# Performance work log

Measured on AMD Instinct MI355X. Metric: run time of the kernel, lower is better.

Reference implementation:

```python
import jax, jax.numpy as jnp
import numpy as np

D = 256
H = 8
HD = D // H  # 32
EPS = 1e-5


def _ln(x, g, b):
    m = jnp.mean(x, axis=-1, keepdims=True)
    v = jnp.var(x, axis=-1, keepdims=True)
    return (x - m) * jax.lax.rsqrt(v + EPS) * g + b


def setup_inputs() -> dict:
    key = jax.random.key(0)
    ks = jax.random.split(key, 30)
    B = 131072
    s = 0.05

    def w(k, shape, scale=s):
        return jax.random.normal(k, shape, dtype=jnp.float32) * scale

    inp = {
        'f24': w(ks[0], (B, D), 1.0),
        'f77': w(ks[1], (B, D), 1.0),
        'fx': w(ks[2], (B, D), 1.0),
        'norm_g': jnp.ones((D,), jnp.float32),
        'norm_b': jnp.zeros((D,), jnp.float32),
        'Wq24': w(ks[3], (D, D)), 'bq24': w(ks[4], (D,)),
        'Wk24': w(ks[5], (D, D)), 'bk24': w(ks[6], (D,)),
        'Wv24': w(ks[7], (D, D)), 'bv24': w(ks[8], (D,)),
        'Wq77': w(ks[9], (D, D)), 'bq77': w(ks[10], (D,)),
        'Wk77': w(ks[11], (D, D)), 'bk77': w(ks[12], (D,)),
        'Wv77': w(ks[13], (D, D)), 'bv77': w(ks[14], (D,)),
        'Wqx': w(ks[15], (D, D)), 'bqx': w(ks[16], (D,)),
        'Wkx': w(ks[17], (D, D)), 'bkx': w(ks[18], (D,)),
        'Wvx': w(ks[19], (D, D)), 'bvx': w(ks[20], (D,)),
        'Wout': w(ks[21], (D, D)), 'bout': w(ks[22], (D,)),
        'radar_w': jnp.ones((3,), jnp.float32),
        'W1': w(ks[23], (D, 4 * D)), 'b1': w(ks[24], (4 * D,)),
        'W2': w(ks[25], (4 * D, D)), 'b2': w(ks[26], (D,)),
        'fnorm_g': jnp.ones((D,), jnp.float32),
        'fnorm_b': jnp.zeros((D,), jnp.float32),
    }
    return inp


def reference(f24, f77, fx, norm_g, norm_b,
              Wq24, bq24, Wk24, bk24, Wv24, bv24,
              Wq77, bq77, Wk77, bk77, Wv77, bv77,
              Wqx, bqx, Wkx, bkx, Wvx, bvx,
              Wout, bout, radar_w, W1, b1, W2, b2,
              fnorm_g, fnorm_b):
    B = f24.shape[0]
    residual = (f24 + f77 + fx) / 3.0
    n24 = _ln(f24, norm_g, norm_b)
    n77 = _ln(f77, norm_g, norm_b)
    nx = _ln(fx, norm_g, norm_b)

    def proj(x, W, b):
        return (x @ W + b).reshape(B, H, HD)

    q24 = proj(n24, Wq24, bq24); k24 = proj(n24, Wk24, bk24); v24 = proj(n24, Wv24, bv24)
    q77 = proj(n77, Wq77, bq77); k77 = proj(n77, Wk77, bk77); v77 = proj(n77, Wv77, bv77)
    qx = proj(nx, Wqx, bqx); kx = proj(nx, Wkx, bkx); vx = proj(nx, Wvx, bvx)

    scale = HD ** (-0.5)

    def att(q, ka, kb):  # [B,H,H] each
        a = jnp.einsum('bhd,bgd->bhg', q, ka) * scale
        b_ = jnp.einsum('bhd,bgd->bhg', q, kb) * scale
        # softmax across the two radar sources (stacked dim), NOT over keys
        return jax.nn.softmax(jnp.stack([a, b_], axis=1), axis=1)

    attn_24 = att(q24, k77, kx)
    attn_77 = att(q77, k24, kx)
    attn_x = att(qx, k24, k77)

    def mix(p, va, vb):  # [B,2,H,H] x [B,H,HD] -> [B, D]
        o = jnp.einsum('bhg,bgd->bhd', p[:, 0], va) + jnp.einsum('bhg,bgd->bhd', p[:, 1], vb)
        return o.reshape(B, D)

    out_24 = mix(attn_24, v77, vx)
    out_77 = mix(attn_77, v24, vx)
    out_x = mix(attn_x, v24, v77)

    rw = jax.nn.softmax(radar_w, axis=0)
    fused = rw[0] * out_24 + rw[1] * out_77 + rw[2] * out_x
    fused = fused @ Wout + bout
    fused = fused + residual
    ff = jax.nn.gelu(fused @ W1 + b1, approximate=False) @ W2 + b2  # dropout = eval identity
    output = _ln(fused + ff, fnorm_g, fnorm_b)
    return output, rw
```

## Files before the change

### kernel.cpp

```cpp
#include <hip/hip_runtime.h>

#define DEV __device__ __forceinline__

typedef float f4_t __attribute__((ext_vector_type(4)));
typedef short v8s  __attribute__((ext_vector_type(8)));

DEV float lo16(unsigned int w){ return __uint_as_float(w << 16); }
DEV float hi16(unsigned int w){ return __uint_as_float(w & 0xffff0000u); }
DEV float b2f(unsigned short u){ return __uint_as_float((unsigned)u << 16); }
DEV unsigned short f2b(float f){
  unsigned int x = __float_as_uint(f);
  x += 0x7fffu + ((x >> 16) & 1u);
  return (unsigned short)(x >> 16);
}
DEV float geluf(float v){ return 0.5f * v * (1.0f + erff(v * 0.7071067811865475f)); }

DEV void gload_lds16(const unsigned short* g, unsigned short* l){
  __builtin_amdgcn_global_load_lds(
      (const __attribute__((address_space(1))) void*)g,
      (__attribute__((address_space(3))) void*)l, 16, 0, 0);
}

#define WAITV(n) asm volatile("s_waitcnt vmcnt(" #n ")" ::: "memory")
#define SBAR()  do{ __builtin_amdgcn_sched_barrier(0); \
                    asm volatile("s_barrier" ::: "memory"); \
                    __builtin_amdgcn_sched_barrier(0); }while(0)

__global__ void k_prep(
    const float* Wq24, const float* Wk24, const float* Wv24,
    const float* Wq77, const float* Wk77, const float* Wv77,
    const float* Wqx,  const float* Wkx,  const float* Wvx,
    const float* bq24, const float* bk24, const float* bv24,
    const float* bq77, const float* bk77, const float* bv77,
    const float* bqx,  const float* bkx,  const float* bvx,
    const float* Wout, const float* W1,   const float* W2,
    const float* radar_w,
    unsigned short* wt_cat, unsigned short* wout_t,
    unsigned short* w1_t, unsigned short* w2_t,
    float* bias_cat, float* rwbuf, float* out_tail)
{
  long idx = (long)blockIdx.x * blockDim.x + threadIdx.x;
  if (idx < 589824){
    int s = (int)(idx / 196608);
    int r = (int)(idx % 196608);
    int ng = r >> 8, k = r & 255;
    int which = ng >> 8, n = ng & 255;
    const float* src;
    switch (s*3 + which){
      case 0: src = Wq24; break;  case 1: src = Wk24; break;  case 2: src = Wv24; break;
      case 3: src = Wq77; break;  case 4: src = Wk77; break;  case 5: src = Wv77; break;
      case 6: src = Wqx;  break;  case 7: src = Wkx;  break;  default: src = Wvx; break;
    }
    wt_cat[idx] = f2b(src[k*256 + n]);
    return;
  }
  idx -= 589824;
  if (idx < 65536){ int n = (int)(idx >> 8), k = (int)(idx & 255);
    wout_t[idx] = f2b(Wout[k*256 + n]); return; }
  idx -= 65536;
  if (idx < 262144){ int n = (int)(idx >> 8), k = (int)(idx & 255);
    w1_t[idx] = f2b(W1[k*1024 + n]); return; }
  idx -= 262144;
  if (idx < 262144){ int n = (int)(idx >> 10), k = (int)(idx & 1023);
    w2_t[idx] = f2b(W2[k*256 + n]); return; }
  idx -= 262144;
  if (idx < 2304){
    int s = (int)(idx / 768), j = (int)(idx % 768);
    int which = j >> 8, jj = j & 255;
    const float* src;
    switch (s*3 + which){
      case 0: src = bq24; break;  case 1: src = bk24; break;  case 2: src = bv24; break;
      case 3: src = bq77; break;  case 4: src = bk77; break;  case 5: src = bv77; break;
      case 6: src = bqx;  break;  case 7: src = bkx;  break;  default: src = bvx; break;
    }
    bias_cat[idx] = src[jj]; return;
  }
  idx -= 2304;
  if (idx < 3){
    float w0 = radar_w[0], w1v = radar_w[1], w2v = radar_w[2];
    float m = fmaxf(w0, fmaxf(w1v, w2v));
    float e0 = __expf(w0-m), e1 = __expf(w1v-m), e2 = __expf(w2v-m);
    float inv = 1.0f/(e0+e1+e2);
    float rw = (idx==0 ? e0 : (idx==1 ? e1 : e2)) * inv;
    rwbuf[idx] = rw; out_tail[idx] = rw;
  }
}

__global__ __launch_bounds__(256) void k_ln3(
    const float* __restrict__ f24, const float* __restrict__ f77, const float* __restrict__ fx,
    const float* __restrict__ gg, const float* __restrict__ bb,
    unsigned short* __restrict__ nbuf, float* __restrict__ resid, int rows)
{
  int wid = threadIdx.x >> 6, lane = threadIdx.x & 63;
  long row = (long)blockIdx.x*4 + wid;
  long base = row*256 + lane*4;
  f4_t x0 = *(const f4_t*)(f24 + base);
  f4_t x1 = *(const f4_t*)(f77 + base);
  f4_t x2 = *(const f4_t*)(fx  + base);
  float s[3], q[3];
  s[0]=x0.x+x0.y+x0.z+x0.w;
  s[1]=x1.x+x1.y+x1.z+x1.w;
  s[2]=x2.x+x2.y+x2.z+x2.w;
  q[0]=fmaf(x0.x,x0.x,fmaf(x0.y,x0.y,fmaf(x0.z,x0.z,x0.w*x0.w)));
  q[1]=fmaf(x1.x,x1.x,fmaf(x1.y,x1.y,fmaf(x1.z,x1.z,x1.w*x1.w)));
  q[2]=fmaf(x2.x,x2.x,fmaf(x2.y,x2.y,fmaf(x2.z,x2.z,x2.w*x2.w)));
  #pragma unroll
  for (int m=1;m<64;m<<=1){
    #pragma unroll
    for (int j=0;j<3;j++){ s[j]+=__shfl_xor(s[j],m); q[j]+=__shfl_xor(q[j],m); }
  }
  f4_t G  = *(const f4_t*)(gg + lane*4);
  f4_t Bv = *(const f4_t*)(bb + lane*4);
  long strm = (long)rows*256;
  {
    float mean = s[0]*(1.0f/256.0f);
    float rstd = rsqrtf(q[0]*(1.0f/256.0f) - mean*mean + 1e-5f);
    ushort4 o;
    o.x=f2b((x0.x-mean)*rstd*G.x+Bv.x); o.y=f2b((x0.y-mean)*rstd*G.y+Bv.y);
    o.z=f2b((x0.z-mean)*rstd*G.z+Bv.z); o.w=f2b((x0.w-mean)*rstd*G.w+Bv.w);
    *(ushort4*)(nbuf + base) = o;
  }
  {
    float mean = s[1]*(1.0f/256.0f);
    float rstd = rsqrtf(q[1]*(1.0f/256.0f) - mean*mean + 1e-5f);
    ushort4 o;
    o.x=f2b((x1.x-mean)*rstd*G.x+Bv.x); o.y=f2b((x1.y-mean)*rstd*G.y+Bv.y);
    o.z=f2b((x1.z-mean)*rstd*G.z+Bv.z); o.w=f2b((x1.w-mean)*rstd*G.w+Bv.w);
    *(ushort4*)(nbuf + strm + base) = o;
  }
  {
    float mean = s[2]*(1.0f/256.0f);
    float rstd = rsqrtf(q[2]*(1.0f/256.0f) - mean*mean + 1e-5f);
    ushort4 o;
    o.x=f2b((x2.x-mean)*rstd*G.x+Bv.x); o.y=f2b((x2.y-mean)*rstd*G.y+Bv.y);
    o.z=f2b((x2.z-mean)*rstd*G.z+Bv.z); o.w=f2b((x2.w-mean)*rstd*G.w+Bv.w);
    *(ushort4*)(nbuf + 2*strm + base) = o;
  }
  f4_t rs;
  rs.x=(x0.x+x1.x+x2.x)*(1.0f/3.0f);
  rs.y=(x0.y+x1.y+x2.y)*(1.0f/3.0f);
  rs.z=(x0.z+x1.z+x2.z)*(1.0f/3.0f);
  rs.w=(x0.w+x1.w+x2.w)*(1.0f/3.0f);
  *(f4_t*)(resid + base) = rs;
}

template<int EPI>
__global__ __launch_bounds__(256,2) void k_gemm256(
    const unsigned short* __restrict__ A, const unsigned short* __restrict__ Bt,
    const float* __restrict__ bias,
    unsigned short* __restrict__ outH,
    long aBatch, long bBatch, long biasBatch, long oBatch, int ldOut,
    int tM, int tN, int tZ)
{
  __shared__ __align__(16) unsigned short As[2][128][64];
  __shared__ __align__(16) unsigned short Bs[2][128][64];
  int tid = threadIdx.x, wid = tid >> 6, lane = tid & 63;
  int wm = (wid >> 1)*64, wn = (wid & 1)*64;
  int lr = lane & 15, lk = lane >> 4;

  int total = tM*tN*tZ;
  int nT = (total - (int)blockIdx.x + (int)gridDim.x - 1) / (int)gridDim.x;
  if (nT <= 0) return;
  int G = nT*4;

  auto tileOf = [&](int j, long& m0, int& n0, int& z){
    int T = (int)blockIdx.x + j*(int)gridDim.x;
    int mt = T % tM; int rest = T / tM;
    int nt = rest % tN; z = rest / tN;
    m0 = (long)mt*128; n0 = nt*128;
  };

  auto stage = [&](int g){
    long m0; int n0, z;
    tileOf(g >> 2, m0, n0, z);
    int k0 = (g & 3)*64, bi = g & 1;
    const unsigned short* Ab = A  + (long)z*aBatch + m0*256;
    const unsigned short* Bb = Bt + (long)z*bBatch + (long)n0*256;
    #pragma unroll
    for (int i=0;i<4;i++){
      int c = (wid*4+i)*64 + lane;
      int r = c >> 3, sl = (c & 7) ^ (r & 7);
      gload_lds16(Ab + (long)r*256 + k0 + sl*8, &As[bi][0][0] + (long)(wid*4+i)*512);
      gload_lds16(Bb + (long)r*256 + k0 + sl*8, &Bs[bi][0][0] + (long)(wid*4+i)*512);
    }
  };

  const f4_t fz = {0.f,0.f,0.f,0.f};
  f4_t acc[4][4] = {};

  stage(0);
  for (int g=0; g<G; ++g){
    if (g+1 < G){ stage(g+1); WAITV(8); }
    else        { WAITV(0); }
    SBAR();
    int cur = g & 1;
    #pragma unroll
    for (int ks=0; ks<2; ++ks){
      v8s af[4], bfv[4];
      #pragma unroll
      for (int f=0; f<4; f++){
        int prA = wm + f*16 + lr;
        int prB = wn + f*16 + lr;
        int js  = ks*4 + lk;
        af[f]  = *(const v8s*)&As[cur][prA][(js ^ (prA & 7))*8];
        bfv[f] = *(const v8s*)&Bs[cur][prB][(js ^ (prB & 7))*8];
      }
      #pragma unroll
      for (int fm=0; fm<4; fm++)
        #pragma unroll
        for (int fn=0; fn<4; fn++)
          acc[fm][fn] = __builtin_amdgcn_mfma_f32_16x16x32_bf16(bfv[fn], af[fm], acc[fm][fn], 0,0,0);
    }
    if ((g & 3) == 3){
      long m0; int n0, z;
      tileOf(g >> 2, m0, n0, z);
      long zo = (long)z*oBatch;
      const float* bp = bias + (long)z*biasBatch;
      #pragma unroll
      for (int fm=0; fm<4; fm++){
        long gm = m0 + wm + fm*16 + lr;
        long rowo = zo + gm*(long)ldOut;
        #pragma unroll
        for (int fn=0; fn<4; fn++){
          int gn = n0 + wn + fn*16 + lk*4;
          f4_t bv = *(const f4_t*)(bp + gn);
          f4_t v = acc[fm][fn];
          v.x += bv.x; v.y += bv.y; v.z += bv.z; v.w += bv.w;
          ushort4 o; o.x=f2b(v.x); o.y=f2b(v.y); o.z=f2b(v.z); o.w=f2b(v.w);
          *(ushort4*)(outH + rowo + gn) = o;
          acc[fm][fn] = fz;
        }
      }
    }
    SBAR();
  }
}

__global__ __launch_bounds__(512,4) void k_attn(
    const unsigned short* __restrict__ qkv, const float* __restrict__ rwb,
    unsigned short* __restrict__ outA, int rows)
{
  __shared__ __align__(16) unsigned short L[8][72][40];
  int tid = threadIdx.x, wid = tid >> 6, lane = tid & 63;
  long brow0 = (long)blockIdx.x * 8;
  for (int c = tid; c < 2304; c += 512){
    int row = c / 288, rem = c % 288;
    int s = rem / 96, cc = rem % 96;
    int vi = cc >> 2, ch = cc & 3;
    const uint4* src = (const uint4*)(qkv + ((long)s*rows + brow0 + row)*768 + cc*8);
    *(uint4*)&L[row][s*24 + vi][ch*8] = *src;
  }
  __syncthreads();

  int h = lane >> 3, g = lane & 7;
  const unsigned short* R = &L[wid][0][0];
  float comb[32];
  #pragma unroll
  for (int i=0;i<32;i++) comb[i] = 0.0f;
  float rw0 = rwb[0], rw1 = rwb[1], rw2 = rwb[2];

  #pragma unroll
  for (int att=0; att<3; ++att){
    int qs  = att;
    int as_ = (att==0) ? 1 : 0;
    int bs_ = (att==2) ? 1 : 2;
    float rwv = (att==0) ? rw0 : ((att==1) ? rw1 : rw2);
    const unsigned short* qp  = R + (qs *24      + h)*40;
    const unsigned short* kap = R + (as_*24 + 8  + g)*40;
    const unsigned short* kbp = R + (bs_*24 + 8  + g)*40;
    float a = 0.0f, b = 0.0f;
    #pragma unroll
    for (int j=0;j<4;j++){
      uint4 qc  = *(const uint4*)(qp  + j*8);
      uint4 kac = *(const uint4*)(kap + j*8);
      uint4 kbc = *(const uint4*)(kbp + j*8);
      #define DOT2(QW,KA,KB) { float q0=lo16(QW), q1=hi16(QW); \
        a=fmaf(q0,lo16(KA),a); a=fmaf(q1,hi16(KA),a); \
        b=fmaf(q0,lo16(KB),b); b=fmaf(q1,hi16(KB),b); }
      DOT2(qc.x, kac.x, kbc.x) DOT2(qc.y, kac.y, kbc.y)
      DOT2(qc.z, kac.z, kbc.z) DOT2(qc.w, kac.w, kbc.w)
      #undef DOT2
    }
    float d  = (b - a) * 0.17677669529663689f;
    float p0 = 1.0f / (1.0f + __expf(d));
    float p1 = 1.0f - p0;
    float w0 = rwv * p0, w1 = rwv * p1;
    const unsigned short* vap = R + (as_*24 + 16 + g)*40;
    const unsigned short* vbp = R + (bs_*24 + 16 + g)*40;
    #pragma unroll
    for (int j=0;j<4;j++){
      uint4 va = *(const uint4*)(vap + j*8);
      uint4 vb = *(const uint4*)(vbp + j*8);
      #define MIX2(VA,VB,C0,C1) { \
        C0 = fmaf(w0, lo16(VA), fmaf(w1, lo16(VB), C0)); \
        C1 = fmaf(w0, hi16(VA), fmaf(w1, hi16(VB), C1)); }
      MIX2(va.x, vb.x, comb[j*8+0], comb[j*8+1])
      MIX2(va.y, vb.y, comb[j*8+2], comb[j*8+3])
      MIX2(va.z, vb.z, comb[j*8+4], comb[j*8+5])
      MIX2(va.w, vb.w, comb[j*8+6], comb[j*8+7])
      #undef MIX2
    }
  }

  float t16[16];
  { bool up = (lane & 4) != 0;
    #pragma unroll
    for (int i=0;i<16;i++){
      float send = up ? comb[i] : comb[16+i];
      float keep = up ? comb[16+i] : comb[i];
      t16[i] = keep + __shfl_xor(send, 4);
    } }
  float t8[8];
  { bool up = (lane & 2) != 0;
    #pragma unroll
    for (int i=0;i<8;i++){
      float send = up ? t16[i] : t16[8+i];
      float keep = up ? t16[8+i] : t16[i];
      t8[i] = keep + __shfl_xor(send, 2);
    } }
  float t4[4];
  { bool up = (lane & 1) != 0;
    #pragma unroll
    for (int i=0;i<4;i++){
      float send = up ? t8[i] : t8[4+i];
      float keep = up ? t8[4+i] : t8[i];
      t4[i] = keep + __shfl_xor(send, 1);
    } }

  long orow = brow0 + wid;
  ushort4 o4;
  o4.x = f2b(t4[0]); o4.y = f2b(t4[1]); o4.z = f2b(t4[2]); o4.w = f2b(t4[3]);
  *(ushort4*)(outA + orow*256 + lane*4) = o4;
}

__global__ __launch_bounds__(256,2) void k_back(
    const unsigned short* __restrict__ attn,
    const float* __restrict__ resid,
    const unsigned short* __restrict__ woutT,
    const unsigned short* __restrict__ w1T,
    const unsigned short* __restrict__ w2T,
    const float* __restrict__ bout, const float* __restrict__ b1,
    const float* __restrict__ b2,
    const float* __restrict__ fg, const float* __restrict__ fb,
    float* __restrict__ dout)
{
  __shared__ __align__(16) unsigned short FL[8192];
  __shared__ __align__(16) unsigned short STG[16384];
  __shared__ __align__(16) unsigned short R2[4096];
  int tid = threadIdx.x, wid = tid >> 6, lane = tid & 63;
  int lr = lane & 15, lk = lane >> 4;
  int wn = wid*64, wnB = wid*32;
  long m0 = (long)blockIdx.x * 32;

  f4_t accA[2][4] = {};
  for (int t=0; t<4; ++t){
    { int c = tid; int r = c>>3, sl = (c&7)^(r&7);
      gload_lds16(attn + (m0+r)*256 + t*64 + sl*8, R2 + c*8); }
    #pragma unroll
    for (int i=0;i<8;i++){ int c = i*256+tid; int r = c>>3, sl = (c&7)^(r&7);
      gload_lds16(woutT + (long)r*256 + t*64 + sl*8, STG + c*8); }
    __syncthreads();
    #pragma unroll
    for (int ks=0; ks<2; ++ks){
      v8s af[2], bf[4];
      #pragma unroll
      for (int f=0; f<2; f++){ int pr = f*16+lr;
        af[f] = *(const v8s*)(R2 + pr*64 + (((ks*4+lk) ^ (pr&7))*8)); }
      #pragma unroll
      for (int f=0; f<4; f++){ int pr = wn + f*16 + lr;
        bf[f] = *(const v8s*)(STG + pr*64 + (((ks*4+lk) ^ (pr&7))*8)); }
      #pragma unroll
      for (int fm=0; fm<2; fm++)
        #pragma unroll
        for (int fn=0; fn<4; fn++)
          accA[fm][fn] = __builtin_amdgcn_mfma_f32_16x16x32_bf16(bf[fn], af[fm], accA[fm][fn], 0,0,0);
    }
    __syncthreads();
  }
  #pragma unroll
  for (int fm=0; fm<2; fm++){
    int row = fm*16 + lr;
    #pragma unroll
    for (int fn=0; fn<4; fn++){
      int col = wn + fn*16 + lk*4;
      f4_t bv = *(const f4_t*)(bout + col);
      f4_t rv = *(const f4_t*)(resid + (m0+row)*256 + col);
      f4_t v = accA[fm][fn];
      v.x += bv.x + rv.x; v.y += bv.y + rv.y; v.z += bv.z + rv.z; v.w += bv.w + rv.w;
      ushort4 hh; hh.x=f2b(v.x); hh.y=f2b(v.y); hh.z=f2b(v.z); hh.w=f2b(v.w);
      int us = row*256 + (((col>>3) ^ (row&7))*8) + (col&7);
      *(ushort4*)(FL + us) = hh;
    }
  }
  __syncthreads();

  f4_t acc2[2][4] = {};
  for (int s=0; s<8; ++s){
    f4_t accH[2][2] = {};
    for (int t=0; t<4; ++t){
      #pragma unroll
      for (int i=0;i<4;i++){ int c = i*256+tid; int r = c>>3, sl = (c&7)^(r&7);
        gload_lds16(w1T + (long)(s*128+r)*256 + t*64 + sl*8, STG + c*8); }
      __syncthreads();
      #pragma unroll
      for (int ks=0; ks<2; ++ks){
        v8s af[2], bf[2];
        #pragma unroll
        for (int f=0; f<2; f++){ int pr = f*16+lr; int ku = t*8 + ks*4 + lk;
          af[f] = *(const v8s*)(FL + pr*256 + ((ku ^ (pr&7))*8)); }
        #pragma unroll
        for (int f=0; f<2; f++){ int pr = wnB + f*16 + lr;
          bf[f] = *(const v8s*)(STG + pr*64 + (((ks*4+lk) ^ (pr&7))*8)); }
        #pragma unroll
        for (int fm=0; fm<2; fm++)
          #pragma unroll
          for (int fn=0; fn<2; fn++)
            accH[fm][fn] = __builtin_amdgcn_mfma_f32_16x16x32_bf16(bf[fn], af[fm], accH[fm][fn], 0,0,0);
      }
      __syncthreads();
    }
    #pragma unroll
    for (int fm=0; fm<2; fm++){
      int row = fm*16 + lr;
      #pragma unroll
      for (int fn=0; fn<2; fn++){
        int col = wnB + fn*16 + lk*4;
        f4_t bv = *(const f4_t*)(b1 + s*128 + col);
        f4_t v = accH[fm][fn];
        v.x = geluf(v.x+bv.x); v.y = geluf(v.y+bv.y);
        v.z = geluf(v.z+bv.z); v.w = geluf(v.w+bv.w);
        ushort4 hh; hh.x=f2b(v.x); hh.y=f2b(v.y); hh.z=f2b(v.z); hh.w=f2b(v.w);
        int us = row*128 + (((col>>3) ^ (row&7))*8) + (col&7);
        *(ushort4*)(R2 + us) = hh;
      }
    }
    __syncthreads();
    for (int t=0; t<2; ++t){
      #pragma unroll
      for (int i=0;i<8;i++){ int c = i*256+tid; int r = c>>3, sl = (c&7)^(r&7);
        gload_lds16(w2T + (long)r*1024 + s*128 + t*64 + sl*8, STG + c*8); }
      __syncthreads();
      #pragma unroll
      for (int ks=0; ks<2; ++ks){
        v8s af[2], bf[4];
        #pragma unroll
        for (int f=0; f<2; f++){ int pr = f*16+lr; int ku = t*8 + ks*4 + lk;
          af[f] = *(const v8s*)(R2 + pr*128 + ((ku ^ (pr&7))*8)); }
        #pragma unroll
        for (int f=0; f<4; f++){ int pr = wn + f*16 + lr;
          bf[f] = *(const v8s*)(STG + pr*64 + (((ks*4+lk) ^ (pr&7))*8)); }
        #pragma unroll
        for (int fm=0; fm<2; fm++)
          #pragma unroll
          for (int fn=0; fn<4; fn++)
            acc2[fm][fn] = __builtin_amdgcn_mfma_f32_16x16x32_bf16(bf[fn], af[fm], acc2[fm][fn], 0,0,0);
      }
      __syncthreads();
    }
  }

  f4_t vv[2][4];
  float ps[2], pq[2];
  #pragma unroll
  for (int fm=0; fm<2; fm++){
    int row = fm*16 + lr;
    ps[fm] = 0.0f; pq[fm] = 0.0f;
    #pragma unroll
    for (int fn=0; fn<4; fn++){
      int col = wn + fn*16 + lk*4;
      f4_t bv = *(const f4_t*)(b2 + col);
      int us = row*256 + (((col>>3) ^ (row&7))*8) + (col&7);
      ushort4 fh = *(const ushort4*)(FL + us);
      f4_t v = acc2[fm][fn];
      v.x += bv.x + b2f(fh.x); v.y += bv.y + b2f(fh.y);
      v.z += bv.z + b2f(fh.z); v.w += bv.w + b2f(fh.w);
      vv[fm][fn] = v;
      ps[fm] += v.x+v.y+v.z+v.w;
      pq[fm] += v.x*v.x + v.y*v.y + v.z*v.z + v.w*v.w;
    }
    ps[fm] += __shfl_xor(ps[fm], 16); ps[fm] += __shfl_xor(ps[fm], 32);
    pq[fm] += __shfl_xor(pq[fm], 16); pq[fm] += __shfl_xor(pq[fm], 32);
  }
  float* PS = (float*)R2;
  float* PQ = (float*)R2 + 128;
  if (lk == 0){
    #pragma unroll
    for (int fm=0; fm<2; fm++){ int row = fm*16+lr;
      PS[row*4 + wid] = ps[fm]; PQ[row*4 + wid] = pq[fm]; }
  }
  __syncthreads();
  #pragma unroll
  for (int fm=0; fm<2; fm++){
    int row = fm*16 + lr;
    f4_t sv = *(const f4_t*)(PS + row*4);
    f4_t qv = *(const f4_t*)(PQ + row*4);
    float S = sv.x+sv.y+sv.z+sv.w, Q = qv.x+qv.y+qv.z+qv.w;
    float mean = S*(1.0f/256.0f);
    float rstd = rsqrtf(Q*(1.0f/256.0f) - mean*mean + 1e-5f);
    #pragma unroll
    for (int fn=0; fn<4; fn++){
      int col = wn + fn*16 + lk*4;
      f4_t G = *(const f4_t*)(fg + col);
      f4_t Bb = *(const f4_t*)(fb + col);
      f4_t v = vv[fm][fn], o;
      o.x = (v.x-mean)*rstd*G.x + Bb.x;
      o.y = (v.y-mean)*rstd*G.y + Bb.y;
      o.z = (v.z-mean)*rstd*G.z + Bb.z;
      o.w = (v.w-mean)*rstd*G.w + Bb.w;
      *(f4_t*)(dout + (m0+row)*256 + col) = o;
    }
  }
}

extern "C" void kernel_launch(void* const* d_in, const int* in_sizes, int n_in,
                              void* d_out, int out_size, void* d_ws, size_t ws_size,
                              hipStream_t stream)
{
  const float* f24    = (const float*)d_in[0];
  const float* f77    = (const float*)d_in[1];
  const float* fx     = (const float*)d_in[2];
  const float* norm_g = (const float*)d_in[3];
  const float* norm_b = (const float*)d_in[4];
  const float* Wq24 = (const float*)d_in[5];  const float* bq24 = (const float*)d_in[6];
  const float* Wk24 = (const float*)d_in[7];  const float* bk24 = (const float*)d_in[8];
  const float* Wv24 = (const float*)d_in[9];  const float* bv24 = (const float*)d_in[10];
  const float* Wq77 = (const float*)d_in[11]; const float* bq77 = (const float*)d_in[12];
  const float* Wk77 = (const float*)d_in[13]; const float* bk77 = (const float*)d_in[14];
  const float* Wv77 = (const float*)d_in[15]; const float* bv77 = (const float*)d_in[16];
  const float* Wqx  = (const float*)d_in[17]; const float* bqx  = (const float*)d_in[18];
  const float* Wkx  = (const float*)d_in[19]; const float* bkx  = (const float*)d_in[20];
  const float* Wvx  = (const float*)d_in[21]; const float* bvx  = (const float*)d_in[22];
  const float* Wout = (const float*)d_in[23]; const float* bout = (const float*)d_in[24];
  const float* radar_w = (const float*)d_in[25];
  const float* W1 = (const float*)d_in[26];   const float* b1 = (const float*)d_in[27];
  const float* W2 = (const float*)d_in[28];   const float* b2 = (const float*)d_in[29];
  const float* fnorm_g = (const float*)d_in[30];
  const float* fnorm_b = (const float*)d_in[31];

  const long Brows = (long)in_sizes[0] / 256;
  float* dout = (float*)d_out;
  char* ws = (char*)d_ws;

  size_t off = 0;
  auto A_ = [&](size_t b){ size_t o = off; off = (off + b + 255) & ~(size_t)255; return o; };
  size_t oWT = A_((size_t)3*768*256*2);
  size_t oWO = A_((size_t)65536*2);
  size_t oW1 = A_((size_t)262144*2);
  size_t oW2 = A_((size_t)262144*2);
  size_t oBC = A_((size_t)2304*4);
  size_t oRW = A_(256);
  size_t fixedEnd = off;

  unsigned short* WT_CAT = (unsigned short*)(ws + oWT);
  unsigned short* WOUT_T = (unsigned short*)(ws + oWO);
  unsigned short* W1_T   = (unsigned short*)(ws + oW1);
  unsigned short* W2_T   = (unsigned short*)(ws + oW2);
  float*          BIASC  = (float*)(ws + oBC);
  float*          RW     = (float*)(ws + oRW);

  const size_t PER_ROW = 7168;
  if (ws_size <= fixedEnd + 512) return;
  long maxR = (long)((ws_size - fixedEnd - 256) / PER_ROW);
  maxR &= ~127L;
  if (maxR < 128) return;
  long Rc = maxR < 65536 ? maxR : 65536;
  if (Rc > Brows) Rc = Brows;
  long nch = (Brows + Rc - 1) / Rc;
  Rc = ((Brows + nch - 1) / nch + 127) & ~127L;

  size_t chunkBase = (fixedEnd + 255) & ~(size_t)255;
  char* NB_B = ws + chunkBase;
  char* RS_B = NB_B + (size_t)1536*Rc;
  char* QK_B = RS_B + (size_t)1024*Rc;

  {
    long total = 589824 + 65536 + 262144 + 262144 + 2304 + 3;
    int blocks = (int)((total + 255) / 256);
    k_prep<<<blocks, 256, 0, stream>>>(
        Wq24, Wk24, Wv24, Wq77, Wk77, Wv77, Wqx, Wkx, Wvx,
        bq24, bk24, bv24, bq77, bk77, bv77, bqx, bkx, bvx,
        Wout, W1, W2, radar_w,
        WT_CAT, WOUT_T, W1_T, W2_T, BIASC, RW, dout + (size_t)Brows*256);
  }

  for (long row0 = 0; row0 < Brows; row0 += Rc){
    long rows = Brows - row0 < Rc ? Brows - row0 : Rc;
    unsigned short* NBUF   = (unsigned short*)NB_B;
    float*          RESID  = (float*)RS_B;
    unsigned short* QKV    = (unsigned short*)QK_B;
    unsigned short* ATTN   = (unsigned short*)NB_B;

    int tM = (int)(rows/128);

    k_ln3<<<(int)(rows/4), 256, 0, stream>>>(
        f24 + row0*256, f77 + row0*256, fx + row0*256,
        norm_g, norm_b, NBUF, RESID, (int)rows);

    { int tiles = tM*6*3; int grid = tiles < 512 ? tiles : 512;
      k_gemm256<0><<<grid, 256, 0, stream>>>(
          NBUF, WT_CAT, BIASC, QKV,
          rows*256L, 768L*256, 768L, rows*768L, 768, tM, 6, 3); }

    k_attn<<<(int)(rows/8), 512, 0, stream>>>(QKV, RW, ATTN, (int)rows);

    k_back<<<(int)(rows/32), 256, 0, stream>>>(
        ATTN, RESID, WOUT_T, W1_T, W2_T,
        bout, b1, b2, fnorm_g, fnorm_b, dout + row0*256);
  }
}
```

Measured before the change: 1.613 ms.

## Make attention kernel persistent with double-buffered async LDS staging, shrink chunk size

The attention kernel becomes a persistent grid-stride loop over 8-row tiles, capped at 512 blocks. It double-buffers tiles in LDS using async global_load_lds so the next tile loads while the current one is computed. The LDS row padding is removed to fit two buffers, and the dot products now use split accumulators. The host row chunk shrinks from 65536 to 16384 rows, which may improve L2 residency of intermediates but adds more launches, and the unpadded layout may cause LDS bank conflicts.

Result: faster. 1.405 ms (-12.9%).

```diff
diff --git a/kernel.cpp b/kernel.cpp
--- a/kernel.cpp
+++ b/kernel.cpp
@@ -240,97 +240,121 @@
     const unsigned short* __restrict__ qkv, const float* __restrict__ rwb,
     unsigned short* __restrict__ outA, int rows)
 {
-  __shared__ __align__(16) unsigned short L[8][72][40];
+  __shared__ __align__(16) unsigned short L[2][8][72][32];
   int tid = threadIdx.x, wid = tid >> 6, lane = tid & 63;
-  long brow0 = (long)blockIdx.x * 8;
-  for (int c = tid; c < 2304; c += 512){
-    int row = c / 288, rem = c % 288;
-    int s = rem / 96, cc = rem % 96;
-    int vi = cc >> 2, ch = cc & 3;
-    const uint4* src = (const uint4*)(qkv + ((long)s*rows + brow0 + row)*768 + cc*8);
-    *(uint4*)&L[row][s*24 + vi][ch*8] = *src;
-  }
-  __syncthreads();
-
+  int nT = rows >> 3;
+  int t0 = blockIdx.x;
+  if (t0 >= nT) return;
+
+  auto stage = [&](int b, int tile){
+    long brow0 = (long)tile*8;
+    unsigned short* Lb = &L[b][0][0][0];
+    #pragma unroll
+    for (int it=0; it<5; ++it){
+      int cw = it*512 + wid*64;
+      if (cw < 2304){
+        int c = cw + lane;
+        int row = c/288, rem = c - row*288;
+        int s = rem/96,  cc  = rem - s*96;
+        gload_lds16(qkv + ((long)s*rows + brow0 + row)*768 + cc*8,
+                    Lb + (long)cw*8);
+      }
+    }
+  };
+
+  float rw0 = rwb[0], rw1 = rwb[1], rw2 = rwb[2];
   int h = lane >> 3, g = lane & 7;
-  const unsigned short* R = &L[wid][0][0];
-  float comb[32];
-  #pragma unroll
-  for (int i=0;i<32;i++) comb[i] = 0.0f;
-  float rw0 = rwb[0], rw1 = rwb[1], rw2 = rwb[2];
-
-  #pragma unroll
-  for (int att=0; att<3; ++att){
-    int qs  = att;
-    int as_ = (att==0) ? 1 : 0;
-    int bs_ = (att==2) ? 1 : 2;
-    float rwv = (att==0) ? rw0 : ((att==1) ? rw1 : rw2);
-    const unsigned short* qp  = R + (qs *24      + h)*40;
-    const unsigned short* kap = R + (as_*24 + 8  + g)*40;
-    const unsigned short* kbp = R + (bs_*24 + 8  + g)*40;
-    float a = 0.0f, b = 0.0f;
-    #pragma unroll
-    for (int j=0;j<4;j++){
-      uint4 qc  = *(const uint4*)(qp  + j*8);
-      uint4 kac = *(const uint4*)(kap + j*8);
-      uint4 kbc = *(const uint4*)(kbp + j*8);
-      #define DOT2(QW,KA,KB) { float q0=lo16(QW), q1=hi16(QW); \
-        a=fmaf(q0,lo16(KA),a); a=fmaf(q1,hi16(KA),a); \
-        b=fmaf(q0,lo16(KB),b); b=fmaf(q1,hi16(KB),b); }
-      DOT2(qc.x, kac.x, kbc.x) DOT2(qc.y, kac.y, kbc.y)
-      DOT2(qc.z, kac.z, kbc.z) DOT2(qc.w, kac.w, kbc.w)
-      #undef DOT2
-    }
-    float d  = (b - a) * 0.17677669529663689f;
-    float p0 = 1.0f / (1.0f + __expf(d));
-    float p1 = 1.0f - p0;
-    float w0 = rwv * p0, w1 = rwv * p1;
-    const unsigned short* vap = R + (as_*24 + 16 + g)*40;
-    const unsigned short* vbp = R + (bs_*24 + 16 + g)*40;
-    #pragma unroll
-    for (int j=0;j<4;j++){
-      uint4 va = *(const uint4*)(vap + j*8);
-      uint4 vb = *(const uint4*)(vbp + j*8);
-      #define MIX2(VA,VB,C0,C1) { \
-        C0 = fmaf(w0, lo16(VA), fmaf(w1, lo16(VB), C0)); \
-        C1 = fmaf(w0, hi16(VA), fmaf(w1, hi16(VB), C1)); }
-      MIX2(va.x, vb.x, comb[j*8+0], comb[j*8+1])
-      MIX2(va.y, vb.y, comb[j*8+2], comb[j*8+3])
-      MIX2(va.z, vb.z, comb[j*8+4], comb[j*8+5])
-      MIX2(va.w, vb.w, comb[j*8+6], comb[j*8+7])
-      #undef MIX2
-    }
-  }
-
-  float t16[16];
-  { bool up = (lane & 4) != 0;
-    #pragma unroll
-    for (int i=0;i<16;i++){
-      float send = up ? comb[i] : comb[16+i];
-      float keep = up ? comb[16+i] : comb[i];
-      t16[i] = keep + __shfl_xor(send, 4);
-    } }
-  float t8[8];
-  { bool up = (lane & 2) != 0;
-    #pragma unroll
-    for (int i=0;i<8;i++){
-      float send = up ? t16[i] : t16[8+i];
-      float keep = up ? t16[8+i] : t16[i];
-      t8[i] = keep + __shfl_xor(send, 2);
-    } }
-  float t4[4];
-  { bool up = (lane & 1) != 0;
-    #pragma unroll
-    for (int i=0;i<4;i++){
-      float send = up ? t8[i] : t8[4+i];
-      float keep = up ? t8[4+i] : t8[i];
-      t4[i] = keep + __shfl_xor(send, 1);
-    } }
-
-  long orow = brow0 + wid;
-  ushort4 o4;
-  o4.x = f2b(t4[0]); o4.y = f2b(t4[1]); o4.z = f2b(t4[2]); o4.w = f2b(t4[3]);
-  *(ushort4*)(outA + orow*256 + lane*4) = o4;
+
+  stage(0, t0);
+  int pb = 0;
+  for (int t = t0; t < nT; t += (int)gridDim.x){
+    SBAR();
+    int tn = t + (int)gridDim.x;
+    if (tn < nT){ stage(pb^1, tn); WAITV(5); }
+    else        { WAITV(0); }
+    SBAR();
+
+    const unsigned short* R = &L[pb][wid][0][0];
+    float comb[32];
+    #pragma unroll
+    for (int i=0;i<32;i++) comb[i] = 0.0f;
+
+    #pragma unroll
+    for (int att=0; att<3; ++att){
+      int qs  = att;
+      int as_ = (att==0) ? 1 : 0;
+      int bs_ = (att==2) ? 1 : 2;
+      float rwv = (att==0) ? rw0 : ((att==1) ? rw1 : rw2);
+      const unsigned short* qp  = R + (qs *24      + h)*32;
+      const unsigned short* kap = R + (as_*24 + 8  + g)*32;
+      const unsigned short* kbp = R + (bs_*24 + 8  + g)*32;
+      float a0=0.f, a1=0.f, b0=0.f, b1=0.f;
+      #pragma unroll
+      for (int j=0;j<4;j++){
+        uint4 qc  = *(const uint4*)(qp  + j*8);
+        uint4 kac = *(const uint4*)(kap + j*8);
+        uint4 kbc = *(const uint4*)(kbp + j*8);
+        float* ap = (j&1) ? &a1 : &a0;
+        float* bp = (j&1) ? &b1 : &b0;
+        #define DOT2(QW,KA,KB) { float q0=lo16(QW), q1=hi16(QW); \
+          *ap=fmaf(q0,lo16(KA),*ap); *ap=fmaf(q1,hi16(KA),*ap); \
+          *bp=fmaf(q0,lo16(KB),*bp); *bp=fmaf(q1,hi16(KB),*bp); }
+        DOT2(qc.x, kac.x, kbc.x) DOT2(qc.y, kac.y, kbc.y)
+        DOT2(qc.z, kac.z, kbc.z) DOT2(qc.w, kac.w, kbc.w)
+        #undef DOT2
+      }
+      float d  = ((b0+b1) - (a0+a1)) * 0.17677669529663689f;
+      float p0 = 1.0f / (1.0f + __expf(d));
+      float p1 = 1.0f - p0;
+      float w0 = rwv * p0, w1 = rwv * p1;
+      const unsigned short* vap = R + (as_*24 + 16 + g)*32;
+      const unsigned short* vbp = R + (bs_*24 + 16 + g)*32;
+      #pragma unroll
+      for (int j=0;j<4;j++){
+        uint4 va = *(const uint4*)(vap + j*8);
+        uint4 vb = *(const uint4*)(vbp + j*8);
+        #define MIX2(VA,VB,C0,C1) { \
+          C0 = fmaf(w0, lo16(VA), fmaf(w1, lo16(VB), C0)); \
+          C1 = fmaf(w0, hi16(VA), fmaf(w1, hi16(VB), C1)); }
+        MIX2(va.x, vb.x, comb[j*8+0], comb[j*8+1])
+        MIX2(va.y, vb.y, comb[j*8+2], comb[j*8+3])
+        MIX2(va.z, vb.z, comb[j*8+4], comb[j*8+5])
+        MIX2(va.w, vb.w, comb[j*8+6], comb[j*8+7])
+        #undef MIX2
+      }
+    }
+
+    float t16[16];
+    { bool up = (lane & 4) != 0;
+      #pragma unroll
+      for (int i=0;i<16;i++){
+        float send = up ? comb[i] : comb[16+i];
+        float keep = up ? comb[16+i] : comb[i];
+        t16[i] = keep + __shfl_xor(send, 4);
+      } }
+    float t8[8];
+    { bool up = (lane & 2) != 0;
+      #pragma unroll
+      for (int i=0;i<8;i++){
+        float send = up ? t16[i] : t16[8+i];
+        float keep = up ? t16[8+i] : t16[i];
+        t8[i] = keep + __shfl_xor(send, 2);
+      } }
+    float t4[4];
+    { bool up = (lane & 1) != 0;
+      #pragma unroll
+      for (int i=0;i<4;i++){
+        float send = up ? t8[i] : t8[4+i];
+        float keep = up ? t8[4+i] : t8[i];
+        t4[i] = keep + __shfl_xor(send, 1);
+      } }
+
+    long orow = (long)t*8 + wid;
+    ushort4 o4;
+    o4.x = f2b(t4[0]); o4.y = f2b(t4[1]); o4.z = f2b(t4[2]); o4.w = f2b(t4[3]);
+    *(ushort4*)(outA + orow*256 + lane*4) = o4;
+    pb ^= 1;
+  }
 }
 
 __global__ __launch_bounds__(256,2) void k_back(
@@ -563,7 +587,7 @@
   long maxR = (long)((ws_size - fixedEnd - 256) / PER_ROW);
   maxR &= ~127L;
   if (maxR < 128) return;
-  long Rc = maxR < 65536 ? maxR : 65536;
+  long Rc = maxR < 16384 ? maxR : 16384;
   if (Rc > Brows) Rc = Brows;
   long nch = (Brows + Rc - 1) / Rc;
   Rc = ((Brows + nch - 1) / nch + 127) & ~127L;
@@ -601,7 +625,8 @@
           NBUF, WT_CAT, BIASC, QKV,
           rows*256L, 768L*256, 768L, rows*768L, 768, tM, 6, 3); }
 
-    k_attn<<<(int)(rows/8), 512, 0, stream>>>(QKV, RW, ATTN, (int)rows);
+    { int nTa = (int)(rows/8); int ga = nTa < 512 ? nTa : 512;
+      k_attn<<<ga, 512, 0, stream>>>(QKV, RW, ATTN, (int)rows); }
 
     k_back<<<(int)(rows/32), 256, 0, stream>>>(
         ATTN, RESID, WOUT_T, W1_T, W2_T,
```
